# Kernel tuning notes

Hardware: AMD Instinct MI355X
Metric: run time of the kernel (lower is better)

The kernel has to match this reference:

```python
import jax, jax.numpy as jnp
import numpy as np

N_NODES = 50000
N_FEAT = 128
HID = 128
OUT = 64


def setup_inputs() -> dict:
    key = jax.random.key(0)
    ks = jax.random.split(key, 16)
    T, N, F, H, O, E = 8, N_NODES, N_FEAT, HID, OUT, 600000
    s = lambda fan: 1.0 / np.sqrt(fan)
    inp = {
        "x_sequence": jax.random.normal(ks[0], (T, N, F), dtype=jnp.float32),
        "edge_index_sequence": jax.random.randint(ks[1], (T, 2, E), 0, N, dtype=jnp.int64),
        # GCN layer 1 and 2 (weight + bias, PyG GCNConv style)
        "W1": jax.random.uniform(ks[2], (F, H), jnp.float32, -s(F), s(F)),
        "b1": jnp.zeros((H,), jnp.float32),
        "W2": jax.random.uniform(ks[3], (H, H), jnp.float32, -s(H), s(H)),
        "b2": jnp.zeros((H,), jnp.float32),
        # LSTM (single layer, gate order i,f,g,o like torch)
        "Wih": jax.random.uniform(ks[4], (4 * H, H), jnp.float32, -s(H), s(H)),
        "Whh": jax.random.uniform(ks[5], (4 * H, H), jnp.float32, -s(H), s(H)),
        "bih": jax.random.uniform(ks[6], (4 * H,), jnp.float32, -s(H), s(H)),
        "bhh": jax.random.uniform(ks[7], (4 * H,), jnp.float32, -s(H), s(H)),
        # output head
        "Wout": jax.random.uniform(ks[8], (H, O), jnp.float32, -s(H), s(H)),
        "bout": jnp.zeros((O,), jnp.float32),
    }
    return inp


def _gcn(x, src, dst, W, b, n_nodes):
    # GCNConv: add self-loops, symmetric normalization D^-1/2 A D^-1/2
    self_idx = jnp.arange(n_nodes)
    s = jnp.concatenate([src, self_idx])
    d = jnp.concatenate([dst, self_idx])
    deg = jax.ops.segment_sum(jnp.ones(s.shape, x.dtype), d, num_segments=n_nodes)
    dinv = jnp.where(deg > 0, jax.lax.rsqrt(deg), 0.0)
    xw = x @ W                                  # [N,H] transform before aggregation
    coef = (dinv[s] * dinv[d])[:, None]         # [E+N,1]
    agg = jax.ops.segment_sum(xw[s] * coef, d, num_segments=n_nodes)
    return agg + b


def reference(x_sequence, edge_index_sequence, W1, b1, W2, b2,
              Wih, Whh, bih, bhh, Wout, bout):
    T, N, F = x_sequence.shape
    H = Whh.shape[1]

    # spatial GCN stack per timestep (dropout is identity at inference)
    def spatial(carry, inp):
        x_t, ei = inp
        src, dst = ei[0], ei[1]
        h = jax.nn.relu(_gcn(x_t, src, dst, W1, b1, N))
        h = jax.nn.relu(_gcn(h, src, dst, W2, b2, N))
        return carry, h

    _, emb = jax.lax.scan(spatial, None, (x_sequence, edge_index_sequence))  # [T,N,H]

    # LSTM over time, batch = N nodes
    def lstm_step(carry, x_t):
        h, c = carry
        g = x_t @ Wih.T + h @ Whh.T + bih + bhh
        i, f, gg, o = jnp.split(g, 4, axis=-1)
        c = jax.nn.sigmoid(f) * c + jax.nn.sigmoid(i) * jnp.tanh(gg)
        h = jax.nn.sigmoid(o) * jnp.tanh(c)
        return (h, c), None

    h0 = jnp.zeros((N, H), x_sequence.dtype)
    c0 = jnp.zeros((N, H), x_sequence.dtype)
    (hT, cT), _ = jax.lax.scan(lstm_step, (h0, c0), emb)

    final = hT                      # lstm_out[:, -1, :] == last hidden state
    output = final @ Wout + bout    # [N, output_dim]
    return output, hT, cT
```

## Files before the change

### kernel.cpp

```cpp
#include <hip/hip_runtime.h>
#include <math.h>

#define TSTEPS 8
#define FDIM 128
#define HDIM 128
#define ODIM 64
#define GDIM 512
#define BUCKR 2048
#define BUCKR_SHIFT 11
#define BPT 32

typedef __attribute__((ext_vector_type(4))) float f32x4;
typedef __attribute__((ext_vector_type(8))) short s8;

__device__ __forceinline__ float sigmf(float x) { return 1.0f / (1.0f + __expf(-x)); }
__device__ __forceinline__ float fast_tanh(float x) {
    float ax = fabsf(x);
    float ez = __expf(2.f * ax);
    float r = 1.f - 2.f / (ez + 1.f);
    return copysignf(r, x);
}

__device__ __forceinline__ ushort f2bf(float x) {
    uint u = __float_as_uint(x);
    u += 0x7FFFu + ((u >> 16) & 1u);
    return (ushort)(u >> 16);
}
__device__ __forceinline__ float bf2f(ushort h) { return __uint_as_float(((uint)h) << 16); }


__global__ void prep_lstm_w(const float* __restrict__ wih, const float* __restrict__ whh,
                            const float* __restrict__ bih, const float* __restrict__ bhh,
                            float* __restrict__ wcat, float* __restrict__ bsum) {
    int idx = blockIdx.x * 256 + threadIdx.x;
    if (idx < 256 * GDIM) {
        int k = idx >> 9;
        int col = idx & 511;
        float v = (k < HDIM) ? wih[col * HDIM + k] : whh[col * HDIM + (k - HDIM)];
        wcat[idx] = v;
        if (k == 0) bsum[col] = bih[col] + bhh[col];
    }
}

__global__ void pack_b(const float* __restrict__ B, int K, int NC,
                       uint* __restrict__ hi, uint* __restrict__ lo) {
    int total = (K / 32) * (NC / 16) * 256;
    int idx = blockIdx.x * 256 + threadIdx.x;
    if (idx >= total) return;
    int d = idx & 3, l = (idx >> 2) & 63, t = idx >> 8;
    int NT = NC / 16;
    int kt = t / NT, nt = t % NT;
    int k = kt * 32 + (l >> 4) * 8 + d * 2;
    int col = nt * 16 + (l & 15);
    float va = B[(size_t)k * NC + col];
    float vb = B[(size_t)(k + 1) * NC + col];
    ushort ha = f2bf(va), hb = f2bf(vb);
    float ra = va - bf2f(ha), rb = vb - bf2f(hb);
    hi[idx] = (uint)ha | ((uint)hb << 16);
    lo[idx] = (uint)f2bf(ra) | ((uint)f2bf(rb) << 16);
}

__global__ void zero_int(int* __restrict__ p, int n) {
    int idx = blockIdx.x * 256 + threadIdx.x;
    if (idx < n) p[idx] = 0;
}


__global__ __launch_bounds__(256) void bin_count(const int* __restrict__ edges,
                                                 int* __restrict__ gcount,
                                                 int E, int N, int nbuck) {
    __shared__ int h[1024];
    int tid = threadIdx.x;
    int t = blockIdx.x >> 5, b = blockIdx.x & 31;
    int ce = (E + BPT - 1) / BPT;
    int e0 = b * ce, e1 = min(e0 + ce, E);
    for (int i = tid; i < 1024; i += 256) h[i] = 0;
    __syncthreads();
    const int* dstp = edges + (size_t)t * 2 * E + E;
    for (int i = e0 + tid; i < e1; i += 256) {
        int gid = t * N + dstp[i];
        atomicAdd(&h[gid >> BUCKR_SHIFT], 1);
    }
    __syncthreads();
    for (int i = tid; i < nbuck; i += 256) {
        int c = h[i];
        if (c) atomicAdd(&gcount[i], c);
    }
}

__global__ __launch_bounds__(1024) void scan_buckets(const int* __restrict__ gcount,
                                                     int* __restrict__ bucket_start,
                                                     int* __restrict__ bucket_cursor,
                                                     int nbuck, int* __restrict__ row_start,
                                                     int nTotal, int totalE) {
    __shared__ int s[1024];
    int t = threadIdx.x;
    int own = (t < nbuck) ? gcount[t] : 0;
    s[t] = own; __syncthreads();
    for (int off = 1; off < 1024; off <<= 1) {
        int add = (t >= off) ? s[t - off] : 0;
        __syncthreads();
        s[t] += add;
        __syncthreads();
    }
    if (t < nbuck) {
        int excl = s[t] - own;
        bucket_start[t] = excl;
        bucket_cursor[t] = excl;
    }
    if (t == 0) {
        bucket_start[nbuck] = totalE;
        row_start[nTotal] = totalE;
    }
}

__global__ __launch_bounds__(256) void bin_scatter(const int* __restrict__ edges,
                                                   int* __restrict__ bucket_cursor,
                                                   uint2* __restrict__ staged,
                                                   int E, int N, int nbuck) {
    __shared__ int h[1024];
    __shared__ int base[1024];
    int tid = threadIdx.x;
    int t = blockIdx.x >> 5, b = blockIdx.x & 31;
    int ce = (E + BPT - 1) / BPT;
    int e0 = b * ce, e1 = min(e0 + ce, E);
    for (int i = tid; i < 1024; i += 256) h[i] = 0;
    __syncthreads();
    const int* srcp = edges + (size_t)t * 2 * E;
    const int* dstp = srcp + E;
    for (int i = e0 + tid; i < e1; i += 256) {
        int gid = t * N + dstp[i];
        atomicAdd(&h[gid >> BUCKR_SHIFT], 1);
    }
    __syncthreads();
    for (int i = tid; i < nbuck; i += 256) {
        int c = h[i];
        if (c) base[i] = atomicAdd(&bucket_cursor[i], c);
        h[i] = 0;
    }
    __syncthreads();
    for (int i = e0 + tid; i < e1; i += 256) {
        int sgid = t * N + srcp[i];
        int dgid = t * N + dstp[i];
        int bk = dgid >> BUCKR_SHIFT;
        int loc = atomicAdd(&h[bk], 1);
        staged[base[bk] + loc] = make_uint2((uint)sgid, (uint)dgid);
    }
}

__global__ __launch_bounds__(256) void bin_csr(const uint2* __restrict__ staged,
                                               const int* __restrict__ bucket_start,
                                               int* __restrict__ row_start,
                                               int* __restrict__ csr_src,
                                               float* __restrict__ dinv, int nTotal) {
    __shared__ int cnt[BUCKR];
    __shared__ int part[256];
    int tid = threadIdx.x;
    int node0 = blockIdx.x << BUCKR_SHIFT;
    int nloc = min(BUCKR, nTotal - node0);
    int ebase = bucket_start[blockIdx.x], eend = bucket_start[blockIdx.x + 1];

    for (int j = tid; j < BUCKR; j += 256) cnt[j] = 0;
    __syncthreads();
    for (int e = ebase + tid; e < eend; e += 256)
        atomicAdd(&cnt[(int)staged[e].y - node0], 1);
    __syncthreads();

    int s = 0;
    #pragma unroll
    for (int k = 0; k < 8; k++) s += cnt[tid * 8 + k];
    part[tid] = s; __syncthreads();
    for (int off = 1; off < 256; off <<= 1) {
        int add = (tid >= off) ? part[tid - off] : 0;
        __syncthreads();
        part[tid] += add;
        __syncthreads();
    }
    int run = part[tid] - s;
    #pragma unroll
    for (int k = 0; k < 8; k++) {
        int j = tid * 8 + k;
        int c = cnt[j];
        if (j < nloc) {
            row_start[node0 + j] = ebase + run;
            dinv[node0 + j] = rsqrtf((float)(c + 1));
        }
        cnt[j] = run;
        run += c;
    }
    __syncthreads();
    for (int e = ebase + tid; e < eend; e += 256) {
        uint2 ed = staged[e];
        int d = (int)ed.y - node0;
        int pos = ebase + atomicAdd(&cnt[d], 1);
        csr_src[pos] = (int)ed.x;
    }
}


__global__ __launch_bounds__(256) void agg_gather_t(
    const int* __restrict__ row_start, const int* __restrict__ csr_src,
    const uint* __restrict__ xh,
    const float* __restrict__ dinv, const float* __restrict__ bias,
    uint* __restrict__ ohi, int rowOff, int outRowOff, int nloc)
{
    int w = (blockIdx.x * 256 + threadIdx.x) >> 6;
    int lane = threadIdx.x & 63;
    if (w >= nloc) return;
    int wg = rowOff + w;
    float dr = dinv[wg];
    float cc = dr * dr;
    uint shv = xh[(size_t)wg * 64 + lane];
    float a0 = __uint_as_float(shv << 16) * cc;
    float a1 = __uint_as_float(shv & 0xFFFF0000u) * cc;
    int e = row_start[wg], e1 = row_start[wg + 1];
    for (; e + 4 <= e1; e += 4) {
        int s0 = csr_src[e], s1 = csr_src[e + 1], s2 = csr_src[e + 2], s3 = csr_src[e + 3];
        float c0 = dinv[s0] * dr, c1 = dinv[s1] * dr, c2 = dinv[s2] * dr, c3 = dinv[s3] * dr;
        uint u0 = xh[(size_t)s0 * 64 + lane];
        uint u1 = xh[(size_t)s1 * 64 + lane];
        uint u2 = xh[(size_t)s2 * 64 + lane];
        uint u3 = xh[(size_t)s3 * 64 + lane];
        a0 = fmaf(__uint_as_float(u0 << 16), c0, a0);
        a1 = fmaf(__uint_as_float(u0 & 0xFFFF0000u), c0, a1);
        a0 = fmaf(__uint_as_float(u1 << 16), c1, a0);
        a1 = fmaf(__uint_as_float(u1 & 0xFFFF0000u), c1, a1);
        a0 = fmaf(__uint_as_float(u2 << 16), c2, a0);
        a1 = fmaf(__uint_as_float(u2 & 0xFFFF0000u), c2, a1);
        a0 = fmaf(__uint_as_float(u3 << 16), c3, a0);
        a1 = fmaf(__uint_as_float(u3 & 0xFFFF0000u), c3, a1);
    }
    for (; e < e1; e++) {
        int s = csr_src[e];
        float cf = dinv[s] * dr;
        uint u = xh[(size_t)s * 64 + lane];
        a0 = fmaf(__uint_as_float(u << 16), cf, a0);
        a1 = fmaf(__uint_as_float(u & 0xFFFF0000u), cf, a1);
    }
    float2 b = ((const float2*)bias)[lane];
    a0 = fmaxf(a0 + b.x, 0.f);
    a1 = fmaxf(a1 + b.y, 0.f);
    ohi[(size_t)(wg - outRowOff) * 64 + lane] = (uint)f2bf(a0) | ((uint)f2bf(a1) << 16);
}


template<bool SPLITSRC>
__global__ __launch_bounds__(512) void gemm_mfma128(
    const float* __restrict__ A32, const ushort* __restrict__ Ahi,
    const uint4* __restrict__ Bhi, const uint4* __restrict__ Blo,
    ushort* __restrict__ Chi, int nrows)
{
    __shared__ ushort AsH[128][136];
    const int r0 = blockIdx.x * 128;
    const int tid = threadIdx.x;

    if (SPLITSRC) {
        for (int v = tid; v < 128 * 16; v += 512) {
            int row = v >> 4, seg = v & 15;
            uint4 h = make_uint4(0, 0, 0, 0);
            if (r0 + row < nrows)
                h = *(const uint4*)(Ahi + (size_t)(r0 + row) * 128 + seg * 8);
            *(uint4*)&AsH[row][seg * 8] = h;
        }
    } else {
        for (int v = tid; v < 128 * 16; v += 512) {
            int row = v >> 4, seg = v & 15;
            float4 a = make_float4(0.f, 0.f, 0.f, 0.f), b = a;
            if (r0 + row < nrows) {
                const float4* src = (const float4*)A32 + (size_t)(r0 + row) * 32 + seg * 2;
                a = src[0]; b = src[1];
            }
            float vv[8] = {a.x, a.y, a.z, a.w, b.x, b.y, b.z, b.w};
            uint hh[4];
            #pragma unroll
            for (int i = 0; i < 4; i++)
                hh[i] = (uint)f2bf(vv[2 * i]) | ((uint)f2bf(vv[2 * i + 1]) << 16);
            *(uint4*)&AsH[row][seg * 8] = make_uint4(hh[0], hh[1], hh[2], hh[3]);
        }
    }
    __syncthreads();

    const int l = tid & 63, w = tid >> 6;
    const int wm = w & 3, wn = w >> 2;
    const int lrow = l & 15, lk = (l >> 4) * 8;

    f32x4 acc[2][4];
    #pragma unroll
    for (int m = 0; m < 2; m++)
        #pragma unroll
        for (int p = 0; p < 4; p++) acc[m][p] = (f32x4){0.f, 0.f, 0.f, 0.f};

    #pragma unroll
    for (int kt = 0; kt < 4; kt++) {
        uint4 BH[4], BL[4];
        #pragma unroll
        for (int p = 0; p < 4; p++) {
            int nt = 4 * wn + p;
            BH[p] = Bhi[(kt * 8 + nt) * 64 + l];
            BL[p] = Blo[(kt * 8 + nt) * 64 + l];
        }
        s8 aH[2];
        #pragma unroll
        for (int m = 0; m < 2; m++) {
            int row = (2 * wm + m) * 16 + lrow;
            aH[m] = *(const s8*)&AsH[row][kt * 32 + lk];
        }
        #pragma unroll
        for (int p = 0; p < 4; p++) {
            s8 bh = __builtin_bit_cast(s8, BH[p]);
            s8 bl = __builtin_bit_cast(s8, BL[p]);
            #pragma unroll
            for (int m = 0; m < 2; m++) {
                acc[m][p] = __builtin_amdgcn_mfma_f32_16x16x32_bf16(aH[m], bh, acc[m][p], 0, 0, 0);
                acc[m][p] = __builtin_amdgcn_mfma_f32_16x16x32_bf16(aH[m], bl, acc[m][p], 0, 0, 0);
            }
        }
    }

    __syncthreads();
    const int lr4 = (l >> 4) * 4;
    #pragma unroll
    for (int m = 0; m < 2; m++) {
        #pragma unroll
        for (int p = 0; p < 4; p++) {
            int col = (4 * wn + p) * 16 + lrow;
            #pragma unroll
            for (int r = 0; r < 4; r++) {
                int row = (2 * wm + m) * 16 + lr4 + r;
                AsH[row][col] = f2bf(acc[m][p][r]);
            }
        }
    }
    __syncthreads();
    for (int v = tid; v < 128 * 16; v += 512) {
        int row = v >> 4, seg = v & 15;
        if (r0 + row < nrows)
            *(uint4*)(Chi + (size_t)(r0 + row) * 128 + seg * 8) = *(const uint4*)&AsH[row][seg * 8];
    }
}


template<bool LAST>
__global__ __launch_bounds__(512, 2) void lstm_step_t(
    const ushort* __restrict__ Ehi, ushort* __restrict__ Hhi,
    const uint4* __restrict__ Bhi, const uint4* __restrict__ Blo,
    const float* __restrict__ bsum, float* __restrict__ cbuf,
    const uint4* __restrict__ Whi, const uint4* __restrict__ Wlo,
    const float* __restrict__ bout,
    float* __restrict__ outp, float* __restrict__ outh, float* __restrict__ outc,
    int nrows)
{
    __shared__ ushort AsH[64][264];
    const int r0 = blockIdx.x * 64;
    const int tid = threadIdx.x;
    const int l = tid & 63, w = tid >> 6;
    const int lrow = l & 15, lk = (l >> 4) * 8, lr4 = (l >> 4) * 4;

    for (int v = tid; v < 64 * 32; v += 512) {
        int row = v >> 5, seg = v & 31;
        uint4 h = make_uint4(0, 0, 0, 0);
        if (r0 + row < nrows) {
            if (seg < 16)
                h = *(const uint4*)(Ehi + (size_t)(r0 + row) * 128 + seg * 8);
            else
                h = *(const uint4*)(Hhi + (size_t)(r0 + row) * 128 + (seg - 16) * 8);
        }
        *(uint4*)&AsH[row][seg * 8] = h;
    }
    __syncthreads();

    f32x4 acc[4][4];
    #pragma unroll
    for (int m = 0; m < 4; m++)
        #pragma unroll
        for (int q = 0; q < 4; q++) {
            float b = bsum[q * 128 + 16 * w + lrow];
            acc[m][q] = (f32x4){b, b, b, b};
        }

    #pragma unroll 2
    for (int kt = 0; kt < 8; kt++) {
        uint4 BH[4], BL[4];
        #pragma unroll
        for (int q = 0; q < 4; q++) {
            int nt = 8 * q + w;
            BH[q] = Bhi[((size_t)kt * 32 + nt) * 64 + l];
            BL[q] = Blo[((size_t)kt * 32 + nt) * 64 + l];
        }
        s8 aH[4];
        #pragma unroll
        for (int m = 0; m < 4; m++) {
            int row = m * 16 + lrow;
            aH[m] = *(const s8*)&AsH[row][kt * 32 + lk];
        }
        #pragma unroll
        for (int q = 0; q < 4; q++) {
            s8 bh = __builtin_bit_cast(s8, BH[q]);
            s8 bl = __builtin_bit_cast(s8, BL[q]);
            #pragma unroll
            for (int m = 0; m < 4; m++) {
                acc[m][q] = __builtin_amdgcn_mfma_f32_16x16x32_bf16(aH[m], bh, acc[m][q], 0, 0, 0);
                acc[m][q] = __builtin_amdgcn_mfma_f32_16x16x32_bf16(aH[m], bl, acc[m][q], 0, 0, 0);
            }
        }
    }
    if (LAST) __syncthreads();

    #pragma unroll
    for (int m = 0; m < 4; m++) {
        int hh = 16 * w + lrow;
        #pragma unroll
        for (int r = 0; r < 4; r++) {
            int row = m * 16 + lr4 + r;
            if (r0 + row < nrows) {
                size_t o = (size_t)(r0 + row) * HDIM + hh;
                float gi = acc[m][0][r], gf = acc[m][1][r];
                float gg = acc[m][2][r], go = acc[m][3][r];
                float cn = sigmf(gf) * cbuf[o] + sigmf(gi) * fast_tanh(gg);
                float hn = sigmf(go) * fast_tanh(cn);
                cbuf[o] = cn;
                ushort hb = f2bf(hn);
                Hhi[o] = hb;
                if (LAST) {
                    outh[o] = hn;
                    outc[o] = cn;
                    AsH[row][128 + hh] = hb;
                }
            }
        }
    }

    if (LAST) {
        __syncthreads();
        if (w < 4) {
            f32x4 hacc[4];
            {
                float b = bout[w * 16 + lrow];
                #pragma unroll
                for (int m = 0; m < 4; m++) hacc[m] = (f32x4){b, b, b, b};
            }
            #pragma unroll
            for (int kt = 0; kt < 4; kt++) {
                uint4 BH = Whi[(kt * 4 + w) * 64 + l];
                uint4 BL = Wlo[(kt * 4 + w) * 64 + l];
                s8 aH[4];
                #pragma unroll
                for (int m = 0; m < 4; m++) {
                    int row = m * 16 + lrow;
                    aH[m] = *(const s8*)&AsH[row][128 + kt * 32 + lk];
                }
                s8 bh = __builtin_bit_cast(s8, BH);
                s8 bl = __builtin_bit_cast(s8, BL);
                #pragma unroll
                for (int m = 0; m < 4; m++) {
                    hacc[m] = __builtin_amdgcn_mfma_f32_16x16x32_bf16(aH[m], bh, hacc[m], 0, 0, 0);
                    hacc[m] = __builtin_amdgcn_mfma_f32_16x16x32_bf16(aH[m], bl, hacc[m], 0, 0, 0);
                }
            }
            #pragma unroll
            for (int m = 0; m < 4; m++) {
                #pragma unroll
                for (int r = 0; r < 4; r++) {
                    int row = r0 + m * 16 + lr4 + r;
                    if (row < nrows)
                        outp[(size_t)row * ODIM + w * 16 + lrow] = hacc[m][r];
                }
            }
        }
    }
}


static inline int cdiv(long long a, long long b) { return (int)((a + b - 1) / b); }

extern "C" void kernel_launch(void* const* d_in, const int* in_sizes, int n_in,
                              void* d_out, int out_size, void* d_ws, size_t ws_size,
                              hipStream_t stream) {
    const float* x_seq = (const float*)d_in[0];
    const int*   edges = (const int*)d_in[1];
    const float* W1    = (const float*)d_in[2];
    const float* b1    = (const float*)d_in[3];
    const float* W2    = (const float*)d_in[4];
    const float* b2    = (const float*)d_in[5];
    const float* Wih   = (const float*)d_in[6];
    const float* Whh   = (const float*)d_in[7];
    const float* bih   = (const float*)d_in[8];
    const float* bhh   = (const float*)d_in[9];
    const float* Wout  = (const float*)d_in[10];
    const float* bout  = (const float*)d_in[11];
    float* out = (float*)d_out;

    const int N = in_sizes[0] / (TSTEPS * FDIM);
    const int E = in_sizes[1] / (2 * TSTEPS);
    const int NT8 = TSTEPS * N;
    const size_t NP = ((size_t)NT8 + 255) & ~(size_t)255;
    const int NBUCK = cdiv(NT8, BUCKR);
    const size_t nf = (size_t)N * FDIM;
    const int E8 = TSTEPS * E;

    float* ws = (float*)d_ws;
    float* dinv = ws;
    float* wcat = dinv + NP;
    float* bsum = wcat + 131072;
    uint* pW1hi = (uint*)(bsum + 512);
    uint* pW1lo = pW1hi + 8192;
    uint* pW2hi = pW1lo + 8192;
    uint* pW2lo = pW2hi + 8192;
    uint* pWchi = pW2lo + 8192;
    uint* pWclo = pWchi + 65536;
    uint* pWohi = pWclo + 65536;
    uint* pWolo = pWohi + 4096;
    float* cbuf = (float*)(pWolo + 4096);
    ushort* hhi = (ushort*)(cbuf + nf);
    ushort* ehi = hhi + nf;
    ushort* xwhi = ehi + nf;
    ushort* h1hi = xwhi + (size_t)NT8 * 128;
    uint2* staged  = (uint2*)(h1hi + (size_t)NT8 * 128);
    int* csr_src   = (int*)(staged + E8);
    int* row_start = csr_src + E8;
    int* gcount    = row_start + NP + 2;
    int* bucket_start  = gcount + 1024;
    int* bucket_cursor = bucket_start + 1026;

    prep_lstm_w<<<cdiv(256 * GDIM, 256), 256, 0, stream>>>(Wih, Whh, bih, bhh, wcat, bsum);
    pack_b<<<32, 256, 0, stream>>>(W1, 128, 128, pW1hi, pW1lo);
    pack_b<<<32, 256, 0, stream>>>(W2, 128, 128, pW2hi, pW2lo);
    pack_b<<<256, 256, 0, stream>>>(wcat, 256, GDIM, pWchi, pWclo);
    pack_b<<<16, 256, 0, stream>>>(Wout, 128, ODIM, pWohi, pWolo);

    zero_int<<<cdiv((long long)nf + nf / 2, 256), 256, 0, stream>>>((int*)cbuf, (int)(nf + nf / 2));

    zero_int<<<4, 256, 0, stream>>>(gcount, 1024);
    bin_count<<<TSTEPS * BPT, 256, 0, stream>>>(edges, gcount, E, N, NBUCK);
    scan_buckets<<<1, 1024, 0, stream>>>(gcount, bucket_start, bucket_cursor, NBUCK,
                                         row_start, NT8, E8);
    bin_scatter<<<TSTEPS * BPT, 256, 0, stream>>>(edges, bucket_cursor, staged, E, N, NBUCK);
    bin_csr<<<NBUCK, 256, 0, stream>>>(staged, bucket_start, row_start, csr_src, dinv, NT8);

    const int gagrid = cdiv((long long)N * 64, 256);

    gemm_mfma128<false><<<cdiv(NT8, 128), 512, 0, stream>>>(
        x_seq, nullptr, (const uint4*)pW1hi, (const uint4*)pW1lo, xwhi, NT8);
    for (int t = 0; t < TSTEPS; t++)
        agg_gather_t<<<gagrid, 256, 0, stream>>>(
            row_start, csr_src, (const uint*)xwhi, dinv, b1,
            (uint*)h1hi, t * N, 0, N);

    gemm_mfma128<true><<<cdiv(NT8, 128), 512, 0, stream>>>(
        nullptr, h1hi, (const uint4*)pW2hi, (const uint4*)pW2lo, xwhi, NT8);

    float* out_h = out + (size_t)N * ODIM;
    float* out_c = out_h + (size_t)N * HDIM;
    for (int t = 0; t < TSTEPS; t++) {
        agg_gather_t<<<gagrid, 256, 0, stream>>>(
            row_start, csr_src, (const uint*)xwhi, dinv, b2,
            (uint*)ehi, t * N, t * N, N);
        if (t < TSTEPS - 1) {
            lstm_step_t<false><<<cdiv(N, 64), 512, 0, stream>>>(
                ehi, hhi, (const uint4*)pWchi, (const uint4*)pWclo, bsum, cbuf,
                nullptr, nullptr, nullptr, nullptr, nullptr, nullptr, N);
        } else {
            lstm_step_t<true><<<cdiv(N, 64), 512, 0, stream>>>(
                ehi, hhi, (const uint4*)pWchi, (const uint4*)pWclo, bsum, cbuf,
                (const uint4*)pWohi, (const uint4*)pWolo, bout,
                out, out_h, out_c, N);
        }
    }
}
```

Baseline: 1.396 ms.

## Fuse LSTM timesteps into two kernels keeping hidden and cell state on-chip

The GCN layer-2 aggregation now runs for all timesteps up front into a full [T,N,H] embedding buffer. The LSTM then runs as two launches of four timesteps each instead of eight. Each launch keeps the cell state in registers and the hidden state in shared memory, writing them to global memory only at its last step. This removes per-step global reads and writes of h and c plus several kernel launches. In exchange the embedding buffer grows to T×N×H and the aggregation no longer interleaves with the LSTM.

```diff
diff --git a/kernel.cpp b/kernel.cpp
--- a/kernel.cpp
+++ b/kernel.cpp
@@ -341,97 +341,122 @@
 
 
 template<bool LAST>
-__global__ __launch_bounds__(512, 2) void lstm_step_t(
-    const ushort* __restrict__ Ehi, ushort* __restrict__ Hhi,
+__global__ __launch_bounds__(512, 2) void lstm_step4(
+    const ushort* __restrict__ Ehi_all,
+    ushort* __restrict__ Hhi,
     const uint4* __restrict__ Bhi, const uint4* __restrict__ Blo,
     const float* __restrict__ bsum, float* __restrict__ cbuf,
     const uint4* __restrict__ Whi, const uint4* __restrict__ Wlo,
     const float* __restrict__ bout,
     float* __restrict__ outp, float* __restrict__ outh, float* __restrict__ outc,
-    int nrows)
+    int tbase, int tcount, int nrows)
 {
     __shared__ ushort AsH[64][264];
     const int r0 = blockIdx.x * 64;
     const int tid = threadIdx.x;
     const int l = tid & 63, w = tid >> 6;
     const int lrow = l & 15, lk = (l >> 4) * 8, lr4 = (l >> 4) * 4;
+    const int hh = 16 * w + lrow;
 
     for (int v = tid; v < 64 * 32; v += 512) {
         int row = v >> 5, seg = v & 31;
         uint4 h = make_uint4(0, 0, 0, 0);
         if (r0 + row < nrows) {
             if (seg < 16)
-                h = *(const uint4*)(Ehi + (size_t)(r0 + row) * 128 + seg * 8);
+                h = *(const uint4*)(Ehi_all + ((size_t)tbase * nrows + r0 + row) * 128 + seg * 8);
             else
                 h = *(const uint4*)(Hhi + (size_t)(r0 + row) * 128 + (seg - 16) * 8);
         }
         *(uint4*)&AsH[row][seg * 8] = h;
     }
-    __syncthreads();
-
-    f32x4 acc[4][4];
+
+    float creg[4][4];
     #pragma unroll
     for (int m = 0; m < 4; m++)
-        #pragma unroll
-        for (int q = 0; q < 4; q++) {
-            float b = bsum[q * 128 + 16 * w + lrow];
-            acc[m][q] = (f32x4){b, b, b, b};
-        }
-
-    #pragma unroll 2
-    for (int kt = 0; kt < 8; kt++) {
-        uint4 BH[4], BL[4];
-        #pragma unroll
-        for (int q = 0; q < 4; q++) {
-            int nt = 8 * q + w;
-            BH[q] = Bhi[((size_t)kt * 32 + nt) * 64 + l];
-            BL[q] = Blo[((size_t)kt * 32 + nt) * 64 + l];
-        }
-        s8 aH[4];
-        #pragma unroll
-        for (int m = 0; m < 4; m++) {
-            int row = m * 16 + lrow;
-            aH[m] = *(const s8*)&AsH[row][kt * 32 + lk];
-        }
-        #pragma unroll
-        for (int q = 0; q < 4; q++) {
-            s8 bh = __builtin_bit_cast(s8, BH[q]);
-            s8 bl = __builtin_bit_cast(s8, BL[q]);
-            #pragma unroll
-            for (int m = 0; m < 4; m++) {
-                acc[m][q] = __builtin_amdgcn_mfma_f32_16x16x32_bf16(aH[m], bh, acc[m][q], 0, 0, 0);
-                acc[m][q] = __builtin_amdgcn_mfma_f32_16x16x32_bf16(aH[m], bl, acc[m][q], 0, 0, 0);
-            }
-        }
-    }
-    if (LAST) __syncthreads();
-
-    #pragma unroll
-    for (int m = 0; m < 4; m++) {
-        int hh = 16 * w + lrow;
         #pragma unroll
         for (int r = 0; r < 4; r++) {
             int row = m * 16 + lr4 + r;
-            if (r0 + row < nrows) {
-                size_t o = (size_t)(r0 + row) * HDIM + hh;
+            creg[m][r] = (r0 + row < nrows) ? cbuf[(size_t)(r0 + row) * HDIM + hh] : 0.f;
+        }
+
+    float bgate[4];
+    #pragma unroll
+    for (int q = 0; q < 4; q++) bgate[q] = bsum[q * 128 + hh];
+
+    __syncthreads();
+
+    #pragma unroll 1
+    for (int ti = 0; ti < tcount; ti++) {
+        f32x4 acc[4][4];
+        #pragma unroll
+        for (int m = 0; m < 4; m++)
+            #pragma unroll
+            for (int q = 0; q < 4; q++)
+                acc[m][q] = (f32x4){bgate[q], bgate[q], bgate[q], bgate[q]};
+
+        #pragma unroll 2
+        for (int kt = 0; kt < 8; kt++) {
+            uint4 BH[4], BL[4];
+            #pragma unroll
+            for (int q = 0; q < 4; q++) {
+                int nt = 8 * q + w;
+                BH[q] = Bhi[((size_t)kt * 32 + nt) * 64 + l];
+                BL[q] = Blo[((size_t)kt * 32 + nt) * 64 + l];
+            }
+            s8 aH[4];
+            #pragma unroll
+            for (int m = 0; m < 4; m++)
+                aH[m] = *(const s8*)&AsH[m * 16 + lrow][kt * 32 + lk];
+            #pragma unroll
+            for (int q = 0; q < 4; q++) {
+                s8 bh = __builtin_bit_cast(s8, BH[q]);
+                s8 bl = __builtin_bit_cast(s8, BL[q]);
+                #pragma unroll
+                for (int m = 0; m < 4; m++) {
+                    acc[m][q] = __builtin_amdgcn_mfma_f32_16x16x32_bf16(aH[m], bh, acc[m][q], 0, 0, 0);
+                    acc[m][q] = __builtin_amdgcn_mfma_f32_16x16x32_bf16(aH[m], bl, acc[m][q], 0, 0, 0);
+                }
+            }
+        }
+        __syncthreads();
+
+        bool lastT = (ti == tcount - 1);
+        #pragma unroll
+        for (int m = 0; m < 4; m++) {
+            #pragma unroll
+            for (int r = 0; r < 4; r++) {
+                int row = m * 16 + lr4 + r;
                 float gi = acc[m][0][r], gf = acc[m][1][r];
                 float gg = acc[m][2][r], go = acc[m][3][r];
-                float cn = sigmf(gf) * cbuf[o] + sigmf(gi) * fast_tanh(gg);
+                float cn = sigmf(gf) * creg[m][r] + sigmf(gi) * fast_tanh(gg);
                 float hn = sigmf(go) * fast_tanh(cn);
-                cbuf[o] = cn;
+                creg[m][r] = cn;
                 ushort hb = f2bf(hn);
-                Hhi[o] = hb;
-                if (LAST) {
-                    outh[o] = hn;
-                    outc[o] = cn;
-                    AsH[row][128 + hh] = hb;
+                AsH[row][128 + hh] = hb;
+                if (r0 + row < nrows) {
+                    size_t o = (size_t)(r0 + row) * HDIM + hh;
+                    if (lastT) {
+                        Hhi[o] = hb;
+                        cbuf[o] = cn;
+                        if (LAST) { outh[o] = hn; outc[o] = cn; }
+                    }
                 }
             }
         }
+        if (!lastT) {
+            int tn = tbase + ti + 1;
+            for (int v = tid; v < 64 * 16; v += 512) {
+                int row = v >> 4, seg = v & 15;
+                uint4 h = make_uint4(0, 0, 0, 0);
+                if (r0 + row < nrows)
+                    h = *(const uint4*)(Ehi_all + ((size_t)tn * nrows + r0 + row) * 128 + seg * 8);
+                *(uint4*)&AsH[row][seg * 8] = h;
+            }
+        }
+        __syncthreads();
     }
 
     if (LAST) {
-        __syncthreads();
         if (w < 4) {
             f32x4 hacc[4];
             {
@@ -445,10 +470,8 @@
                 uint4 BL = Wlo[(kt * 4 + w) * 64 + l];
                 s8 aH[4];
                 #pragma unroll
-                for (int m = 0; m < 4; m++) {
-                    int row = m * 16 + lrow;
-                    aH[m] = *(const s8*)&AsH[row][128 + kt * 32 + lk];
-                }
+                for (int m = 0; m < 4; m++)
+                    aH[m] = *(const s8*)&AsH[m * 16 + lrow][128 + kt * 32 + lk];
                 s8 bh = __builtin_bit_cast(s8, BH);
                 s8 bl = __builtin_bit_cast(s8, BL);
                 #pragma unroll
@@ -513,7 +536,7 @@
     float* cbuf = (float*)(pWolo + 4096);
     ushort* hhi = (ushort*)(cbuf + nf);
     ushort* ehi = hhi + nf;
-    ushort* xwhi = ehi + nf;
+    ushort* xwhi = ehi + (size_t)NT8 * 128;
     ushort* h1hi = xwhi + (size_t)NT8 * 128;
     uint2* staged  = (uint2*)(h1hi + (size_t)NT8 * 128);
     int* csr_src   = (int*)(staged + E8);
@@ -549,21 +572,18 @@
     gemm_mfma128<true><<<cdiv(NT8, 128), 512, 0, stream>>>(
         nullptr, h1hi, (const uint4*)pW2hi, (const uint4*)pW2lo, xwhi, NT8);
 
+    for (int t = 0; t < TSTEPS; t++)
+        agg_gather_t<<<gagrid, 256, 0, stream>>>(
+            row_start, csr_src, (const uint*)xwhi, dinv, b2,
+            (uint*)ehi, t * N, 0, N);
+
     float* out_h = out + (size_t)N * ODIM;
     float* out_c = out_h + (size_t)N * HDIM;
-    for (int t = 0; t < TSTEPS; t++) {
-        agg_gather_t<<<gagrid, 256, 0, stream>>>(
-            row_start, csr_src, (const uint*)xwhi, dinv, b2,
-            (uint*)ehi, t * N, t * N, N);
-        if (t < TSTEPS - 1) {
-            lstm_step_t<false><<<cdiv(N, 64), 512, 0, stream>>>(
-                ehi, hhi, (const uint4*)pWchi, (const uint4*)pWclo, bsum, cbuf,
-                nullptr, nullptr, nullptr, nullptr, nullptr, nullptr, N);
-        } else {
-            lstm_step_t<true><<<cdiv(N, 64), 512, 0, stream>>>(
-                ehi, hhi, (const uint4*)pWchi, (const uint4*)pWclo, bsum, cbuf,
-                (const uint4*)pWohi, (const uint4*)pWolo, bout,
-                out, out_h, out_c, N);
-        }
-    }
-}
+    lstm_step4<false><<<cdiv(N, 64), 512, 0, stream>>>(
+        ehi, hhi, (const uint4*)pWchi, (const uint4*)pWclo, bsum, cbuf,
+        nullptr, nullptr, nullptr, nullptr, nullptr, nullptr, 0, 4, N);
+    lstm_step4<true><<<cdiv(N, 64), 512, 0, stream>>>(
+        ehi, hhi, (const uint4*)pWchi, (const uint4*)pWclo, bsum, cbuf,
+        (const uint4*)pWohi, (const uint4*)pWolo, bout,
+        out, out_h, out_c, 4, 4, N);
+}
```

New measurement: 1.446 ms. +3.6%, slower.
